# Kernel tuning notes

Hardware: AMD Instinct MI355X
Metric: run time of the kernel (lower is better)

The kernel has to match this reference:

```python
import jax, jax.numpy as jnp
import numpy as np

NTYPES = 2
MAXNEI = 128      # maxNeighborNum
M2 = 16
NPER = 256        # atoms per type
B = 4
EMB = [25, 50, 100]
FIT_IN = M2 * EMB[-1]  # 1600
FH = 240


def setup_inputs() -> dict:
    key = jax.random.key(0)
    ks = jax.random.split(key, 16)
    s = 0.1
    inp = {
        "Ri": jax.random.normal(ks[0], (B, NTYPES * NPER, NTYPES * MAXNEI, 4), jnp.float32),
        "emb_W0": jax.random.normal(ks[1], (4, 1, EMB[0]), jnp.float32) * s,
        "emb_b0": jax.random.normal(ks[2], (4, EMB[0]), jnp.float32) * s,
        "emb_W1": jax.random.normal(ks[3], (4, EMB[0], EMB[1]), jnp.float32) * s,
        "emb_b1": jax.random.normal(ks[4], (4, EMB[1]), jnp.float32) * s,
        "emb_W2": jax.random.normal(ks[5], (4, EMB[1], EMB[2]), jnp.float32) * s,
        "emb_b2": jax.random.normal(ks[6], (4, EMB[2]), jnp.float32) * s,
        "fit_W0": jax.random.normal(ks[7], (2, FIT_IN, FH), jnp.float32) * 0.02,
        "fit_b0": jax.random.normal(ks[8], (2, FH), jnp.float32) * s,
        "fit_W1": jax.random.normal(ks[9], (2, FH, FH), jnp.float32) * 0.05,
        "fit_b1": jax.random.normal(ks[10], (2, FH), jnp.float32) * s,
        "fit_W2": jax.random.normal(ks[11], (2, FH, FH), jnp.float32) * 0.05,
        "fit_b2": jax.random.normal(ks[12], (2, FH), jnp.float32) * s,
        "fit_W3": jax.random.normal(ks[13], (2, FH, 1), jnp.float32) * 0.05,
        "fit_b3": jax.random.normal(ks[14], (2, 1), jnp.float32),
    }
    return inp


def _emb(s, W0, b0, W1, b1, W2, b2):
    # DeepMD-style embedding MLP with doubling resnet skips (1->25->50->100)
    h0 = jnp.tanh(s @ W0 + b0)
    h1 = jnp.tanh(h0 @ W1 + b1) + jnp.concatenate([h0, h0], axis=-1)
    h2 = jnp.tanh(h1 @ W2 + b2) + jnp.concatenate([h1, h1], axis=-1)
    return h2


def _fit(d, W0, b0, W1, b1, W2, b2, W3, b3):
    h = jnp.tanh(d @ W0 + b0)
    h = jnp.tanh(h @ W1 + b1) + h   # resnet skip (equal dims)
    h = jnp.tanh(h @ W2 + b2) + h
    return h @ W3 + b3              # [B, N, 1]


def reference(Ri, emb_W0, emb_b0, emb_W1, emb_b1, emb_W2, emb_b2,
              fit_W0, fit_b0, fit_W1, fit_b1, fit_W2, fit_b2, fit_W3, fit_b3):
    type_nums = NTYPES
    Ei_blocks = []
    for i in range(NTYPES):                      # center-atom type
        Ri_i = Ri[:, i * NPER:(i + 1) * NPER]    # [B, NPER, NTYPES*M, 4]
        xyz = None
        for j in range(NTYPES):                  # neighbor type
            blk = Ri_i[:, :, j * MAXNEI:(j + 1) * MAXNEI, :]  # [B,N,M,4]
            S = blk[..., 0:1]                                  # [B,N,M,1]
            e = i * NTYPES + j
            G = _emb(S, emb_W0[e], emb_b0[e], emb_W1[e], emb_b1[e],
                     emb_W2[e], emb_b2[e])                     # [B,N,M,100]
            tmp = jnp.einsum('bnmc,bnmg->bncg', blk, G)        # [B,N,4,100]
            xyz = tmp if xyz is None else xyz + tmp
        xyz = xyz / (MAXNEI * type_nums)
        xyz_b = xyz[..., :M2]                                  # [B,N,4,16]
        DR = jnp.einsum('bncg,bnch->bngh', xyz, xyz_b)         # [B,N,100,16]
        DR = DR.reshape(B, NPER, FIT_IN)
        Ei_i = _fit(DR, fit_W0[i], fit_b0[i], fit_W1[i], fit_b1[i],
                    fit_W2[i], fit_b2[i], fit_W3[i], fit_b3[i])  # [B,N,1]
        Ei_blocks.append(Ei_i)
    Ei = jnp.concatenate(Ei_blocks, axis=1)     # [B, natoms_sum, 1]
    return Ei[..., 0]                            # per-atom energies [B, natoms_sum]
```

## Files before the change

kernel.cpp:

```cpp
#include <hip/hip_runtime.h>
#include <hip/hip_bf16.h>

#define FH 240
#define FIT_IN 1600
#define NK 2048
#define TLO -16.0f
#define TINVH 64.0f

typedef _Float16 h8 __attribute__((ext_vector_type(8)));
typedef float f4v __attribute__((ext_vector_type(4)));

__device__ __forceinline__ float fast_tanh(float x) {
    float e2 = __builtin_amdgcn_exp2f(x * 2.8853900817779268f);
    return 1.0f - 2.0f * __builtin_amdgcn_rcpf(e2 + 1.0f);
}

#define FMA_ROW(r, s) \
    acc[r][0] += (s) * b0.x; acc[r][1] += (s) * b0.y; \
    acc[r][2] += (s) * b0.z; acc[r][3] += (s) * b0.w; \
    acc[r][4] += (s) * b1.x; acc[r][5] += (s) * b1.y; \
    acc[r][6] += (s) * b1.z; acc[r][7] += (s) * b1.w;

#define TOFF_W0   0
#define TOFF_B0   28
#define TOFF_B1   56
#define TOFF_B2   108
#define TOFF_W1   208
#define TOFF_W2   1508
#define TOFF_H0T  6708
#define TOFF_H1T  10008
#define TSMEM     16608

__global__ __launch_bounds__(256) void k_prep(
    const float* __restrict__ eW0, const float* __restrict__ eB0,
    const float* __restrict__ eW1, const float* __restrict__ eB1,
    const float* __restrict__ eW2, const float* __restrict__ eB2,
    float* __restrict__ T,
    const float* __restrict__ fW0, const float* __restrict__ fW1,
    const float* __restrict__ fW2,
    _Float16* __restrict__ W0T, _Float16* __restrict__ W1T,
    _Float16* __restrict__ W2T)
{
    const int bx = blockIdx.x;
    const int t  = threadIdx.x;

    if (bx >= 64) {
        const int total = 768000 + 115200 + 115200;
        for (int idx = (bx - 64) * 256 + t; idx < total; idx += 64 * 256) {
            if (idx < 768000) {
                const int tp = idx / 384000, r = idx - tp * 384000;
                const int k = r / 240, n = r - k * 240;
                W0T[tp * 384000 + n * 1600 + k] = (_Float16)fW0[idx];
            } else if (idx < 883200) {
                const int j = idx - 768000;
                const int tp = j / 57600, r = j - tp * 57600;
                const int k = r / 240, n = r - k * 240;
                W1T[tp * 57600 + n * 240 + k] = (_Float16)fW1[j];
            } else {
                const int j = idx - 883200;
                const int tp = j / 57600, r = j - tp * 57600;
                const int k = r / 240, n = r - k * 240;
                W2T[tp * 57600 + n * 240 + k] = (_Float16)fW2[j];
            }
        }
        return;
    }

    __shared__ float sm[TSMEM];
    const int w    = t >> 6;
    const int lane = t & 63;
    const int mi   = lane & 7;
    const int gi   = lane >> 3;
    const int mrow = w * 32 + mi * 4;

    const int e  = bx >> 4;
    const int k0 = (bx & 15) * 128;

    for (int idx = t; idx < 1250; idx += 256) {
        int k = idx / 50, g = idx - k * 50;
        sm[TOFF_W1 + k * 52 + g] = eW1[e * 1250 + idx];
    }
    for (int idx = t; idx < 5000; idx += 256) {
        int k = idx / 100, r = idx - k * 100;
        int half = r / 50, g = r - half * 50;
        sm[TOFF_W2 + k * 104 + half * 52 + g] = eW2[e * 5000 + idx];
    }
    if (t < 25)       { sm[TOFF_W0 + t] = eW0[e * 25 + t]; sm[TOFF_B0 + t] = eB0[e * 25 + t]; }
    else if (t < 75)  { sm[TOFF_B1 + (t - 25)] = eB1[e * 50 + (t - 25)]; }
    else if (t < 175) { sm[TOFF_B2 + (t - 75)] = eB2[e * 100 + (t - 75)]; }
    __syncthreads();

    if (t < 128) {
        const float S = TLO + (float)(k0 + t) * (1.0f / TINVH);
        #pragma unroll
        for (int k = 0; k < 25; ++k)
            sm[TOFF_H0T + k * 132 + t] = fast_tanh(S * sm[TOFF_W0 + k] + sm[TOFF_B0 + k]);
    }
    __syncthreads();

    {
        float acc[4][8];
        #pragma unroll
        for (int r = 0; r < 4; ++r)
            #pragma unroll
            for (int c = 0; c < 8; ++c) acc[r][c] = 0.f;

        #pragma unroll 5
        for (int k = 0; k < 25; ++k) {
            const float4 av = *(const float4*)&sm[TOFF_H0T + k * 132 + mrow];
            const float4 b0 = *(const float4*)&sm[TOFF_W1 + k * 52 + gi * 8];
            const float4 b1 = *(const float4*)&sm[TOFF_W1 + k * 52 + gi * 8 + 4];
            FMA_ROW(0, av.x) FMA_ROW(1, av.y) FMA_ROW(2, av.z) FMA_ROW(3, av.w)
        }
        #pragma unroll
        for (int c = 0; c < 8; ++c) {
            const int g = gi * 8 + c;
            if (g < 50) {
                const int gm = (g < 25) ? g : g - 25;
                const float4 h0r = *(const float4*)&sm[TOFF_H0T + gm * 132 + mrow];
                const float bias = sm[TOFF_B1 + g];
                float4 o;
                o.x = fast_tanh(acc[0][c] + bias) + h0r.x;
                o.y = fast_tanh(acc[1][c] + bias) + h0r.y;
                o.z = fast_tanh(acc[2][c] + bias) + h0r.z;
                o.w = fast_tanh(acc[3][c] + bias) + h0r.w;
                *(float4*)&sm[TOFF_H1T + g * 132 + mrow] = o;
            }
        }
    }
    __syncthreads();

    for (int half = 0; half < 2; ++half) {
        float acc[4][8];
        #pragma unroll
        for (int r = 0; r < 4; ++r)
            #pragma unroll
            for (int c = 0; c < 8; ++c) acc[r][c] = 0.f;

        #pragma unroll 5
        for (int k = 0; k < 50; ++k) {
            const float4 av = *(const float4*)&sm[TOFF_H1T + k * 132 + mrow];
            const float4 b0 = *(const float4*)&sm[TOFF_W2 + k * 104 + half * 52 + gi * 8];
            const float4 b1 = *(const float4*)&sm[TOFF_W2 + k * 104 + half * 52 + gi * 8 + 4];
            FMA_ROW(0, av.x) FMA_ROW(1, av.y) FMA_ROW(2, av.z) FMA_ROW(3, av.w)
        }
        #pragma unroll
        for (int c = 0; c < 8; ++c) {
            const int g = gi * 8 + c;
            if (g < 50) {
                const float4 h1r = *(const float4*)&sm[TOFF_H1T + g * 132 + mrow];
                const float bias = sm[TOFF_B2 + half * 50 + g];
                float* out = T + ((size_t)e * NK + k0 + mrow) * 100 + half * 50 + g;
                out[0]   = fast_tanh(acc[0][c] + bias) + h1r.x;
                out[100] = fast_tanh(acc[1][c] + bias) + h1r.y;
                out[200] = fast_tanh(acc[2][c] + bias) + h1r.z;
                out[300] = fast_tanh(acc[3][c] + bias) + h1r.w;
            }
        }
    }
}

__global__ __launch_bounds__(256) void k_xyz(
    const float* __restrict__ Ri, const float* __restrict__ T,
    _Float16* __restrict__ DRh)
{
    __shared__ float4 sR[256];
    __shared__ float  sF[256];
    __shared__ int    sI[256];
    __shared__ float  sXYZ[400];

    const int t    = threadIdx.x;
    const int w    = t >> 6;
    const int lane = t & 63;
    const int blk  = blockIdx.x;
    const int b    = blk >> 9;
    const int i    = (blk >> 8) & 1;
    const int n    = blk & 255;

    for (int idx = t; idx < 400; idx += 256) sXYZ[idx] = 0.f;

    {
        const int jj = t >> 7, m = t & 127;
        const size_t row = ((size_t)(b * 512 + i * 256 + n)) * 256 + jj * 128 + m;
        const float4 r = *(const float4*)(Ri + row * 4);
        sR[t] = r;
        float u = (r.x - TLO) * TINVH;
        int ii = (int)u;
        ii = (ii < 0) ? 0 : ((ii > NK - 2) ? NK - 2 : ii);
        sI[t] = ii;
        sF[t] = u - (float)ii;
    }
    __syncthreads();

    float a0[4] = {0.f, 0.f, 0.f, 0.f};
    float a1[4] = {0.f, 0.f, 0.f, 0.f};

    for (int jj = 0; jj < 2; ++jj) {
        const float* Te = T + (size_t)(i * 2 + jj) * NK * 100;
        #pragma unroll 4
        for (int mm = 0; mm < 32; ++mm) {
            const int s = jj * 128 + (w << 5) + mm;
            const int row = sI[s];
            const float f = sF[s];
            const float4 R = sR[s];
            const float* p = Te + (size_t)row * 100;
            const float v0 = p[lane], v1 = p[100 + lane];
            const float G = v0 + f * (v1 - v0);
            a0[0] += R.x * G; a0[1] += R.y * G; a0[2] += R.z * G; a0[3] += R.w * G;
            if (lane < 36) {
                const float u0 = p[64 + lane], u1 = p[164 + lane];
                const float G2 = u0 + f * (u1 - u0);
                a1[0] += R.x * G2; a1[1] += R.y * G2; a1[2] += R.z * G2; a1[3] += R.w * G2;
            }
        }
    }

    #pragma unroll
    for (int c = 0; c < 4; ++c) atomicAdd(&sXYZ[c * 100 + lane], a0[c]);
    if (lane < 36) {
        #pragma unroll
        for (int c = 0; c < 4; ++c) atomicAdd(&sXYZ[c * 100 + 64 + lane], a1[c]);
    }
    __syncthreads();

    const float inv = 1.0f / 65536.0f;
    _Float16* dr = DRh + (((size_t)i * 4 + b) * 256 + n) * FIT_IN;
    for (int q = t; q < 400; q += 256) {
        const int gg = q >> 2, h0 = (q & 3) * 4;
        ushort4 pk;
        _Float16* ph = (_Float16*)&pk;
        #pragma unroll
        for (int r = 0; r < 4; ++r) {
            const int h = h0 + r;
            const float v = (sXYZ[gg] * sXYZ[h] + sXYZ[100 + gg] * sXYZ[100 + h]
                           + sXYZ[200 + gg] * sXYZ[200 + h] + sXYZ[300 + gg] * sXYZ[300 + h]) * inv;
            ph[r] = (_Float16)v;
        }
        *(ushort4*)(dr + gg * 16 + h0) = pk;
    }
}

__global__ __launch_bounds__(256) void k_fit0(
    const _Float16* __restrict__ A, const _Float16* __restrict__ WT,
    float* __restrict__ P)
{
    constexpr int K = FIT_IN, CHUNK = 200;
    __shared__ _Float16 sA[32 * 40];
    __shared__ _Float16 sBT[240 * 40];

    const int t    = threadIdx.x;
    const int w    = t >> 6;
    const int lane = t & 63;
    const int ln   = lane & 15;
    const int quad = lane >> 4;

    const int mtile = blockIdx.x;
    const int ks    = blockIdx.y;
    const int row0  = mtile * 32;
    const int tp    = mtile >> 5;
    const int kbeg  = ks * CHUNK, kend = kbeg + CHUNK;
    const int nf0   = w * 4;

    f4v acc[2][4];
    #pragma unroll
    for (int mf = 0; mf < 2; ++mf)
        #pragma unroll
        for (int nf = 0; nf < 4; ++nf) acc[mf][nf] = (f4v)0.f;

    const _Float16* Ab = A + (size_t)row0 * K;
    const _Float16* Wb = WT + (size_t)tp * 240 * K;

    for (int k0 = kbeg; k0 < kend; k0 += 32) {
        {
            const int m = t >> 3, kq = (t & 7) * 4;
            const int k = k0 + kq;
            uint2 v = make_uint2(0u, 0u);
            if (k < kend) v = *(const uint2*)(Ab + (size_t)m * K + k);
            *(uint2*)&sA[m * 40 + kq] = v;
        }
        for (int q = t; q < 1920; q += 256) {
            const int nn = q >> 3, kq = (q & 7) * 4;
            const int k = k0 + kq;
            uint2 v = make_uint2(0u, 0u);
            if (k < kend) v = *(const uint2*)(Wb + (size_t)nn * K + k);
            *(uint2*)&sBT[nn * 40 + kq] = v;
        }
        __syncthreads();

        h8 afr[2];
        #pragma unroll
        for (int mf = 0; mf < 2; ++mf)
            afr[mf] = *(const h8*)&sA[(mf * 16 + ln) * 40 + quad * 8];
        #pragma unroll
        for (int nf = 0; nf < 4; ++nf) {
            const int n15 = nf0 + nf;
            if (n15 < 15) {
                const h8 bfr = *(const h8*)&sBT[(n15 * 16 + ln) * 40 + quad * 8];
                #pragma unroll
                for (int mf = 0; mf < 2; ++mf)
                    acc[mf][nf] = __builtin_amdgcn_mfma_f32_16x16x32_f16(
                        afr[mf], bfr, acc[mf][nf], 0, 0, 0);
            }
        }
        __syncthreads();
    }

    float* Pb = P + ((size_t)ks * 2048 + row0) * FH;
    #pragma unroll
    for (int nf = 0; nf < 4; ++nf) {
        const int n15 = nf0 + nf;
        if (n15 < 15) {
            const int col = n15 * 16 + ln;
            #pragma unroll
            for (int mf = 0; mf < 2; ++mf)
                #pragma unroll
                for (int r = 0; r < 4; ++r)
                    Pb[(size_t)(mf * 16 + quad * 4 + r) * FH + col] = acc[mf][nf][r];
        }
    }
}

__global__ __launch_bounds__(256) void k_fit_reduce(
    const float* __restrict__ P, const float* __restrict__ Bias,
    float* __restrict__ OutF, _Float16* __restrict__ OutH)
{
    const int idx = blockIdx.x * 256 + threadIdx.x;
    if (idx >= 2048 * FH) return;
    const int tp  = idx / (1024 * FH);
    const int col = idx % FH;
    float s = 0.f;
    #pragma unroll
    for (int ks = 0; ks < 8; ++ks)
        s += P[(size_t)ks * 2048 * FH + idx];
    const float v = fast_tanh(s + Bias[tp * FH + col]);
    OutF[idx] = v;
    OutH[idx] = (_Float16)v;
}

__global__ __launch_bounds__(256) void k_fit_layer(
    const _Float16* __restrict__ Ah, const _Float16* __restrict__ WT,
    const float* __restrict__ Bias, const float* __restrict__ ResF,
    float* __restrict__ OutF, _Float16* __restrict__ OutH)
{
    __shared__ _Float16 sA[16 * 264];
    __shared__ _Float16 sBT[240 * 40];

    const int t    = threadIdx.x;
    const int w    = t >> 6;
    const int lane = t & 63;
    const int ln   = lane & 15;
    const int quad = lane >> 4;

    const int m0 = blockIdx.x * 16;
    const int tp = m0 >> 10;
    const int nf0 = w * 4;

    for (int q = t; q < 1056; q += 256) {
        const int m = q / 66, kq = (q - m * 66) * 4;
        uint2 v = make_uint2(0u, 0u);
        if (kq < 240) v = *(const uint2*)(Ah + (size_t)(m0 + m) * 240 + kq);
        *(uint2*)&sA[m * 264 + kq] = v;
    }

    const _Float16* Wb = WT + (size_t)tp * 240 * 240;

    f4v acc[4];
    #pragma unroll
    for (int nf = 0; nf < 4; ++nf) acc[nf] = (f4v)0.f;

    for (int k0 = 0; k0 < 240; k0 += 32) {
        for (int q = t; q < 1920; q += 256) {
            const int nn = q >> 3, kq = (q & 7) * 4;
            const int k = k0 + kq;
            uint2 v = make_uint2(0u, 0u);
            if (k < 240) v = *(const uint2*)(Wb + (size_t)nn * 240 + k);
            *(uint2*)&sBT[nn * 40 + kq] = v;
        }
        __syncthreads();

        const h8 afr = *(const h8*)&sA[ln * 264 + k0 + quad * 8];
        #pragma unroll
        for (int nf = 0; nf < 4; ++nf) {
            const int n15 = nf0 + nf;
            if (n15 < 15) {
                const h8 bfr = *(const h8*)&sBT[(n15 * 16 + ln) * 40 + quad * 8];
                acc[nf] = __builtin_amdgcn_mfma_f32_16x16x32_f16(afr, bfr, acc[nf], 0, 0, 0);
            }
        }
        __syncthreads();
    }

    #pragma unroll
    for (int nf = 0; nf < 4; ++nf) {
        const int n15 = nf0 + nf;
        if (n15 < 15) {
            const int col = n15 * 16 + ln;
            #pragma unroll
            for (int r = 0; r < 4; ++r) {
                const int row = quad * 4 + r;
                const size_t o = (size_t)(m0 + row) * FH + col;
                const float v = fast_tanh(acc[nf][r] + Bias[tp * FH + col]) + ResF[o];
                OutF[o] = v;
                OutH[o] = (_Float16)v;
            }
        }
    }
}

__global__ __launch_bounds__(256) void k_fit_last(
    const _Float16* __restrict__ Ah, const _Float16* __restrict__ WT,
    const float* __restrict__ Bias, const float* __restrict__ ResF,
    const float* __restrict__ W3, const float* __restrict__ b3,
    float* __restrict__ out)
{
    __shared__ _Float16 sA[16 * 264];
    __shared__ _Float16 sBT[240 * 40];
    __shared__ float sH[16 * 244];
    __shared__ float sW3[240];

    const int t    = threadIdx.x;
    const int w    = t >> 6;
    const int lane = t & 63;
    const int ln   = lane & 15;
    const int quad = lane >> 4;

    const int m0 = blockIdx.x * 16;
    const int tp = m0 >> 10;
    const int nf0 = w * 4;

    for (int q = t; q < 1056; q += 256) {
        const int m = q / 66, kq = (q - m * 66) * 4;
        uint2 v = make_uint2(0u, 0u);
        if (kq < 240) v = *(const uint2*)(Ah + (size_t)(m0 + m) * 240 + kq);
        *(uint2*)&sA[m * 264 + kq] = v;
    }
    if (t < 240) sW3[t] = W3[tp * 240 + t];

    const _Float16* Wb = WT + (size_t)tp * 240 * 240;

    f4v acc[4];
    #pragma unroll
    for (int nf = 0; nf < 4; ++nf) acc[nf] = (f4v)0.f;

    for (int k0 = 0; k0 < 240; k0 += 32) {
        for (int q = t; q < 1920; q += 256) {
            const int nn = q >> 3, kq = (q & 7) * 4;
            const int k = k0 + kq;
            uint2 v = make_uint2(0u, 0u);
            if (k < 240) v = *(const uint2*)(Wb + (size_t)nn * 240 + k);
            *(uint2*)&sBT[nn * 40 + kq] = v;
        }
        __syncthreads();

        const h8 afr = *(const h8*)&sA[ln * 264 + k0 + quad * 8];
        #pragma unroll
        for (int nf = 0; nf < 4; ++nf) {
            const int n15 = nf0 + nf;
            if (n15 < 15) {
                const h8 bfr = *(const h8*)&sBT[(n15 * 16 + ln) * 40 + quad * 8];
                acc[nf] = __builtin_amdgcn_mfma_f32_16x16x32_f16(afr, bfr, acc[nf], 0, 0, 0);
            }
        }
        __syncthreads();
    }

    #pragma unroll
    for (int nf = 0; nf < 4; ++nf) {
        const int n15 = nf0 + nf;
        if (n15 < 15) {
            const int col = n15 * 16 + ln;
            #pragma unroll
            for (int r = 0; r < 4; ++r) {
                const int row = quad * 4 + r;
                sH[row * 244 + col] = fast_tanh(acc[nf][r] + Bias[tp * FH + col])
                                    + ResF[(size_t)(m0 + row) * FH + col];
            }
        }
    }
    __syncthreads();

    #pragma unroll
    for (int rr = 0; rr < 4; ++rr) {
        const int row = w * 4 + rr;
        float s = 0.f;
        for (int c = lane; c < 240; c += 64) s += sH[row * 244 + c] * sW3[c];
        #pragma unroll
        for (int off = 32; off > 0; off >>= 1) s += __shfl_down(s, off);
        if (lane == 0) {
            const int g = m0 + row;
            const int rem = g & 1023;
            const int bb = rem >> 8, nn = rem & 255;
            out[bb * 512 + tp * 256 + nn] = s + b3[tp];
        }
    }
}

extern "C" void kernel_launch(void* const* d_in, const int* in_sizes, int n_in,
                              void* d_out, int out_size, void* d_ws, size_t ws_size,
                              hipStream_t stream)
{
    const float* Ri  = (const float*)d_in[0];
    const float* eW0 = (const float*)d_in[1];
    const float* eB0 = (const float*)d_in[2];
    const float* eW1 = (const float*)d_in[3];
    const float* eB1 = (const float*)d_in[4];
    const float* eW2 = (const float*)d_in[5];
    const float* eB2 = (const float*)d_in[6];
    const float* fW0 = (const float*)d_in[7];
    const float* fb0 = (const float*)d_in[8];
    const float* fW1 = (const float*)d_in[9];
    const float* fb1 = (const float*)d_in[10];
    const float* fW2 = (const float*)d_in[11];
    const float* fb2 = (const float*)d_in[12];
    const float* fW3 = (const float*)d_in[13];
    const float* fb3 = (const float*)d_in[14];

    char* p = (char*)d_ws;
    float* T      = (float*)p;      p += (size_t)4 * NK * 100 * 4;
    float* P      = (float*)p;      p += (size_t)8 * 2048 * FH * 4;
    float* hA     = (float*)p;      p += (size_t)2048 * FH * 4;
    float* hB     = (float*)p;      p += (size_t)2048 * FH * 4;
    _Float16* DRh = (_Float16*)p;   p += (size_t)2048 * FIT_IN * 2;
    _Float16* hAh = (_Float16*)p;   p += (size_t)2048 * FH * 2;
    _Float16* hBh = (_Float16*)p;   p += (size_t)2048 * FH * 2;
    _Float16* W0T = (_Float16*)p;   p += (size_t)768000 * 2;
    _Float16* W1T = (_Float16*)p;   p += (size_t)115200 * 2;
    _Float16* W2T = (_Float16*)p;   p += (size_t)115200 * 2;

    const int RBLK = (2048 * FH + 255) / 256;

    k_prep<<<dim3(128), dim3(256), 0, stream>>>(eW0, eB0, eW1, eB1, eW2, eB2, T,
                                                fW0, fW1, fW2, W0T, W1T, W2T);
    k_xyz<<<dim3(2048), dim3(256), 0, stream>>>(Ri, T, DRh);

    k_fit0<<<dim3(64, 8), dim3(256), 0, stream>>>(DRh, W0T, P);
    k_fit_reduce<<<dim3(RBLK), dim3(256), 0, stream>>>(P, fb0, hA, hAh);

    k_fit_layer<<<dim3(128), dim3(256), 0, stream>>>(hAh, W1T, fb1, hA, hB, hBh);
    k_fit_last<<<dim3(128), dim3(256), 0, stream>>>(hBh, W2T, fb2, hB, fW3, fb3,
                                                    (float*)d_out);
}
```

Before: 210.9 us.

## Store embedding table as interleaved fp16 pairs and fuse fitting tail kernels

The embedding lookup table is now stored in fp16, with each entry packed next to its successor row's value. One 32-bit load then gives both interpolation endpoints, which halves the gather traffic in k_xyz. Separately, the split-K reduction, both hidden fitting layers and the final dot product are merged into one kernel that keeps activations in shared memory. This removes three launches and the global round trips for the intermediates. The costs are reduced precision in the table and 128 blocks doing serial work inside the fused kernel.

```diff
diff --git a/kernel.cpp b/kernel.cpp
--- a/kernel.cpp
+++ b/kernel.cpp
@@ -8,6 +8,7 @@
 #define TINVH 64.0f
 
 typedef _Float16 h8 __attribute__((ext_vector_type(8)));
+typedef _Float16 h2v __attribute__((ext_vector_type(2)));
 typedef float f4v __attribute__((ext_vector_type(4)));
 
 __device__ __forceinline__ float fast_tanh(float x) {
@@ -35,7 +36,7 @@
     const float* __restrict__ eW0, const float* __restrict__ eB0,
     const float* __restrict__ eW1, const float* __restrict__ eB1,
     const float* __restrict__ eW2, const float* __restrict__ eB2,
-    float* __restrict__ T,
+    ushort* __restrict__ Tp,
     const float* __restrict__ fW0, const float* __restrict__ fW1,
     const float* __restrict__ fW2,
     _Float16* __restrict__ W0T, _Float16* __restrict__ W1T,
@@ -150,18 +151,28 @@
             if (g < 50) {
                 const float4 h1r = *(const float4*)&sm[TOFF_H1T + g * 132 + mrow];
                 const float bias = sm[TOFF_B2 + half * 50 + g];
-                float* out = T + ((size_t)e * NK + k0 + mrow) * 100 + half * 50 + g;
-                out[0]   = fast_tanh(acc[0][c] + bias) + h1r.x;
-                out[100] = fast_tanh(acc[1][c] + bias) + h1r.y;
-                out[200] = fast_tanh(acc[2][c] + bias) + h1r.z;
-                out[300] = fast_tanh(acc[3][c] + bias) + h1r.w;
+                const int col = half * 50 + g;
+                float vv[4];
+                vv[0] = fast_tanh(acc[0][c] + bias) + h1r.x;
+                vv[1] = fast_tanh(acc[1][c] + bias) + h1r.y;
+                vv[2] = fast_tanh(acc[2][c] + bias) + h1r.z;
+                vv[3] = fast_tanh(acc[3][c] + bias) + h1r.w;
+                #pragma unroll
+                for (int r = 0; r < 4; ++r) {
+                    const int kk = k0 + mrow + r;
+                    const _Float16 hf = (_Float16)vv[r];
+                    const ushort hs = *(const ushort*)&hf;
+                    const size_t base = ((size_t)e * NK + kk) * 100 + col;
+                    Tp[2 * base] = hs;
+                    if (kk > 0) Tp[2 * base - 199] = hs;
+                }
             }
         }
     }
 }
 
 __global__ __launch_bounds__(256) void k_xyz(
-    const float* __restrict__ Ri, const float* __restrict__ T,
+    const float* __restrict__ Ri, const ushort* __restrict__ Tp,
     _Float16* __restrict__ DRh)
 {
     __shared__ float4 sR[256];
@@ -196,20 +207,22 @@
     float a1[4] = {0.f, 0.f, 0.f, 0.f};
 
     for (int jj = 0; jj < 2; ++jj) {
-        const float* Te = T + (size_t)(i * 2 + jj) * NK * 100;
-        #pragma unroll 4
+        const h2v* Te = (const h2v*)Tp + (size_t)(i * 2 + jj) * NK * 100;
+        #pragma unroll 8
         for (int mm = 0; mm < 32; ++mm) {
             const int s = jj * 128 + (w << 5) + mm;
             const int row = sI[s];
             const float f = sF[s];
             const float4 R = sR[s];
-            const float* p = Te + (size_t)row * 100;
-            const float v0 = p[lane], v1 = p[100 + lane];
-            const float G = v0 + f * (v1 - v0);
+            const h2v* p = Te + (size_t)row * 100;
+            const h2v hv = p[lane];
+            const float v0 = (float)hv[0];
+            const float G = v0 + f * ((float)hv[1] - v0);
             a0[0] += R.x * G; a0[1] += R.y * G; a0[2] += R.z * G; a0[3] += R.w * G;
             if (lane < 36) {
-                const float u0 = p[64 + lane], u1 = p[164 + lane];
-                const float G2 = u0 + f * (u1 - u0);
+                const h2v hu = p[64 + lane];
+                const float u0 = (float)hu[0];
+                const float G2 = u0 + f * ((float)hu[1] - u0);
                 a1[0] += R.x * G2; a1[1] += R.y * G2; a1[2] += R.z * G2; a1[3] += R.w * G2;
             }
         }
@@ -320,30 +333,17 @@
     }
 }
 
-__global__ __launch_bounds__(256) void k_fit_reduce(
-    const float* __restrict__ P, const float* __restrict__ Bias,
-    float* __restrict__ OutF, _Float16* __restrict__ OutH)
+__global__ __launch_bounds__(256) void k_fit_tail(
+    const float* __restrict__ P, const float* __restrict__ b0,
+    const _Float16* __restrict__ W1T, const float* __restrict__ b1,
+    const _Float16* __restrict__ W2T, const float* __restrict__ b2,
+    const float* __restrict__ W3, const float* __restrict__ b3,
+    float* __restrict__ out)
 {
-    const int idx = blockIdx.x * 256 + threadIdx.x;
-    if (idx >= 2048 * FH) return;
-    const int tp  = idx / (1024 * FH);
-    const int col = idx % FH;
-    float s = 0.f;
-    #pragma unroll
-    for (int ks = 0; ks < 8; ++ks)
-        s += P[(size_t)ks * 2048 * FH + idx];
-    const float v = fast_tanh(s + Bias[tp * FH + col]);
-    OutF[idx] = v;
-    OutH[idx] = (_Float16)v;
-}
-
-__global__ __launch_bounds__(256) void k_fit_layer(
-    const _Float16* __restrict__ Ah, const _Float16* __restrict__ WT,
-    const float* __restrict__ Bias, const float* __restrict__ ResF,
-    float* __restrict__ OutF, _Float16* __restrict__ OutH)
-{
-    __shared__ _Float16 sA[16 * 264];
+    __shared__ float    sAf[16 * 240];
+    __shared__ _Float16 sA16[16 * 264];
     __shared__ _Float16 sBT[240 * 40];
+    __shared__ float    sW3[240];
 
     const int t    = threadIdx.x;
     const int w    = t >> 6;
@@ -355,135 +355,82 @@
     const int tp = m0 >> 10;
     const int nf0 = w * 4;
 
-    for (int q = t; q < 1056; q += 256) {
-        const int m = q / 66, kq = (q - m * 66) * 4;
-        uint2 v = make_uint2(0u, 0u);
-        if (kq < 240) v = *(const uint2*)(Ah + (size_t)(m0 + m) * 240 + kq);
-        *(uint2*)&sA[m * 264 + kq] = v;
-    }
-
-    const _Float16* Wb = WT + (size_t)tp * 240 * 240;
-
-    f4v acc[4];
-    #pragma unroll
-    for (int nf = 0; nf < 4; ++nf) acc[nf] = (f4v)0.f;
-
-    for (int k0 = 0; k0 < 240; k0 += 32) {
-        for (int q = t; q < 1920; q += 256) {
-            const int nn = q >> 3, kq = (q & 7) * 4;
-            const int k = k0 + kq;
-            uint2 v = make_uint2(0u, 0u);
-            if (k < 240) v = *(const uint2*)(Wb + (size_t)nn * 240 + k);
-            *(uint2*)&sBT[nn * 40 + kq] = v;
-        }
-        __syncthreads();
-
-        const h8 afr = *(const h8*)&sA[ln * 264 + k0 + quad * 8];
+    {
+        const int mr = t >> 4, c0 = t & 15;
+        #pragma unroll
+        for (int it = 0; it < 15; ++it) {
+            const int c = c0 + it * 16;
+            float s = 0.f;
+            #pragma unroll
+            for (int ks = 0; ks < 8; ++ks)
+                s += P[(size_t)ks * 2048 * FH + (size_t)(m0 + mr) * FH + c];
+            const float v = fast_tanh(s + b0[tp * FH + c]);
+            sAf[mr * 240 + c] = v;
+            sA16[mr * 264 + c] = (_Float16)v;
+        }
+        sA16[mr * 264 + 240 + c0] = (_Float16)0.f;
+        if (c0 < 8) sA16[mr * 264 + 256 + c0] = (_Float16)0.f;
+    }
+    if (t < 240) sW3[t] = W3[tp * FH + t];
+    __syncthreads();
+
+    for (int layer = 0; layer < 2; ++layer) {
+        const _Float16* Wb = (layer == 0 ? W1T : W2T) + (size_t)tp * 240 * 240;
+        const float* Bias  = (layer == 0 ? b1 : b2);
+
+        f4v acc[4];
+        #pragma unroll
+        for (int nf = 0; nf < 4; ++nf) acc[nf] = (f4v)0.f;
+
+        for (int k0 = 0; k0 < 240; k0 += 32) {
+            for (int q = t; q < 1920; q += 256) {
+                const int nn = q >> 3, kq = (q & 7) * 4;
+                const int k = k0 + kq;
+                uint2 v = make_uint2(0u, 0u);
+                if (k < 240) v = *(const uint2*)(Wb + (size_t)nn * 240 + k);
+                *(uint2*)&sBT[nn * 40 + kq] = v;
+            }
+            __syncthreads();
+
+            const h8 afr = *(const h8*)&sA16[ln * 264 + k0 + quad * 8];
+            #pragma unroll
+            for (int nf = 0; nf < 4; ++nf) {
+                const int n15 = nf0 + nf;
+                if (n15 < 15) {
+                    const h8 bfr = *(const h8*)&sBT[(n15 * 16 + ln) * 40 + quad * 8];
+                    acc[nf] = __builtin_amdgcn_mfma_f32_16x16x32_f16(afr, bfr, acc[nf], 0, 0, 0);
+                }
+            }
+            __syncthreads();
+        }
+
         #pragma unroll
         for (int nf = 0; nf < 4; ++nf) {
             const int n15 = nf0 + nf;
             if (n15 < 15) {
-                const h8 bfr = *(const h8*)&sBT[(n15 * 16 + ln) * 40 + quad * 8];
-                acc[nf] = __builtin_amdgcn_mfma_f32_16x16x32_f16(afr, bfr, acc[nf], 0, 0, 0);
+                const int col = n15 * 16 + ln;
+                #pragma unroll
+                for (int r = 0; r < 4; ++r) {
+                    const int row = quad * 4 + r;
+                    const float v = fast_tanh(acc[nf][r] + Bias[tp * FH + col])
+                                  + sAf[row * 240 + col];
+                    sAf[row * 240 + col] = v;
+                    sA16[row * 264 + col] = (_Float16)v;
+                }
             }
         }
         __syncthreads();
     }
-
-    #pragma unroll
-    for (int nf = 0; nf < 4; ++nf) {
-        const int n15 = nf0 + nf;
-        if (n15 < 15) {
-            const int col = n15 * 16 + ln;
-            #pragma unroll
-            for (int r = 0; r < 4; ++r) {
-                const int row = quad * 4 + r;
-                const size_t o = (size_t)(m0 + row) * FH + col;
-                const float v = fast_tanh(acc[nf][r] + Bias[tp * FH + col]) + ResF[o];
-                OutF[o] = v;
-                OutH[o] = (_Float16)v;
-            }
-        }
-    }
-}
-
-__global__ __launch_bounds__(256) void k_fit_last(
-    const _Float16* __restrict__ Ah, const _Float16* __restrict__ WT,
-    const float* __restrict__ Bias, const float* __restrict__ ResF,
-    const float* __restrict__ W3, const float* __restrict__ b3,
-    float* __restrict__ out)
-{
-    __shared__ _Float16 sA[16 * 264];
-    __shared__ _Float16 sBT[240 * 40];
-    __shared__ float sH[16 * 244];
-    __shared__ float sW3[240];
-
-    const int t    = threadIdx.x;
-    const int w    = t >> 6;
-    const int lane = t & 63;
-    const int ln   = lane & 15;
-    const int quad = lane >> 4;
-
-    const int m0 = blockIdx.x * 16;
-    const int tp = m0 >> 10;
-    const int nf0 = w * 4;
-
-    for (int q = t; q < 1056; q += 256) {
-        const int m = q / 66, kq = (q - m * 66) * 4;
-        uint2 v = make_uint2(0u, 0u);
-        if (kq < 240) v = *(const uint2*)(Ah + (size_t)(m0 + m) * 240 + kq);
-        *(uint2*)&sA[m * 264 + kq] = v;
-    }
-    if (t < 240) sW3[t] = W3[tp * 240 + t];
-
-    const _Float16* Wb = WT + (size_t)tp * 240 * 240;
-
-    f4v acc[4];
-    #pragma unroll
-    for (int nf = 0; nf < 4; ++nf) acc[nf] = (f4v)0.f;
-
-    for (int k0 = 0; k0 < 240; k0 += 32) {
-        for (int q = t; q < 1920; q += 256) {
-            const int nn = q >> 3, kq = (q & 7) * 4;
-            const int k = k0 + kq;
-            uint2 v = make_uint2(0u, 0u);
-            if (k < 240) v = *(const uint2*)(Wb + (size_t)nn * 240 + k);
-            *(uint2*)&sBT[nn * 40 + kq] = v;
-        }
-        __syncthreads();
-
-        const h8 afr = *(const h8*)&sA[ln * 264 + k0 + quad * 8];
-        #pragma unroll
-        for (int nf = 0; nf < 4; ++nf) {
-            const int n15 = nf0 + nf;
-            if (n15 < 15) {
-                const h8 bfr = *(const h8*)&sBT[(n15 * 16 + ln) * 40 + quad * 8];
-                acc[nf] = __builtin_amdgcn_mfma_f32_16x16x32_f16(afr, bfr, acc[nf], 0, 0, 0);
-            }
-        }
-        __syncthreads();
-    }
-
-    #pragma unroll
-    for (int nf = 0; nf < 4; ++nf) {
-        const int n15 = nf0 + nf;
-        if (n15 < 15) {
-            const int col = n15 * 16 + ln;
-            #pragma unroll
-            for (int r = 0; r < 4; ++r) {
-                const int row = quad * 4 + r;
-                sH[row * 244 + col] = fast_tanh(acc[nf][r] + Bias[tp * FH + col])
-                                    + ResF[(size_t)(m0 + row) * FH + col];
-            }
-        }
-    }
-    __syncthreads();
 
     #pragma unroll
     for (int rr = 0; rr < 4; ++rr) {
         const int row = w * 4 + rr;
         float s = 0.f;
-        for (int c = lane; c < 240; c += 64) s += sH[row * 244 + c] * sW3[c];
+        #pragma unroll
+        for (int it = 0; it < 4; ++it) {
+            const int c = lane + it * 64;
+            if (c < 240) s += sAf[row * 240 + c] * sW3[c];
+        }
         #pragma unroll
         for (int off = 32; off > 0; off >>= 1) s += __shfl_down(s, off);
         if (lane == 0) {
@@ -516,27 +463,17 @@
     const float* fb3 = (const float*)d_in[14];
 
     char* p = (char*)d_ws;
-    float* T      = (float*)p;      p += (size_t)4 * NK * 100 * 4;
     float* P      = (float*)p;      p += (size_t)8 * 2048 * FH * 4;
-    float* hA     = (float*)p;      p += (size_t)2048 * FH * 4;
-    float* hB     = (float*)p;      p += (size_t)2048 * FH * 4;
+    ushort* Tp    = (ushort*)p;     p += (size_t)4 * NK * 100 * 4;
     _Float16* DRh = (_Float16*)p;   p += (size_t)2048 * FIT_IN * 2;
-    _Float16* hAh = (_Float16*)p;   p += (size_t)2048 * FH * 2;
-    _Float16* hBh = (_Float16*)p;   p += (size_t)2048 * FH * 2;
     _Float16* W0T = (_Float16*)p;   p += (size_t)768000 * 2;
     _Float16* W1T = (_Float16*)p;   p += (size_t)115200 * 2;
     _Float16* W2T = (_Float16*)p;   p += (size_t)115200 * 2;
 
-    const int RBLK = (2048 * FH + 255) / 256;
-
-    k_prep<<<dim3(128), dim3(256), 0, stream>>>(eW0, eB0, eW1, eB1, eW2, eB2, T,
+    k_prep<<<dim3(128), dim3(256), 0, stream>>>(eW0, eB0, eW1, eB1, eW2, eB2, Tp,
                                                 fW0, fW1, fW2, W0T, W1T, W2T);
-    k_xyz<<<dim3(2048), dim3(256), 0, stream>>>(Ri, T, DRh);
-
+    k_xyz<<<dim3(2048), dim3(256), 0, stream>>>(Ri, Tp, DRh);
     k_fit0<<<dim3(64, 8), dim3(256), 0, stream>>>(DRh, W0T, P);
-    k_fit_reduce<<<dim3(RBLK), dim3(256), 0, stream>>>(P, fb0, hA, hAh);
-
-    k_fit_layer<<<dim3(128), dim3(256), 0, stream>>>(hAh, W1T, fb1, hA, hB, hBh);
-    k_fit_last<<<dim3(128), dim3(256), 0, stream>>>(hBh, W2T, fb2, hB, fW3, fb3,
-                                                    (float*)d_out);
-}
+    k_fit_tail<<<dim3(128), dim3(256), 0, stream>>>(P, fb0, W1T, fb1, W2T, fb2,
+                                                    fW3, fb3, (float*)d_out);
+}
```

After: 208.3 us. About the same (-1.2%).
